# Kernel tuning notes

Hardware: AMD Instinct MI355X
Metric: run time of the kernel (lower is better)

## Reference

```python
import jax, jax.numpy as jnp
import numpy as np

V, L, D, C = 50000, 512, 300, 128
KS = (3, 4, 5)
B = 64


def setup_inputs() -> dict:
    key = jax.random.key(0)
    ks = jax.random.split(key, 12)
    inp = {
        "x": jax.random.randint(ks[0], (B, L), 0, V),
        "embed_w": jax.random.normal(ks[1], (V, D), jnp.float32) * 0.1,
        "conv_w": jax.random.normal(ks[2], (C, D), jnp.float32) * 0.05,
        "conv_b": jax.random.normal(ks[3], (C,), jnp.float32) * 0.05,
        "fc3_w": jax.random.normal(ks[4], (L - 3,), jnp.float32) * 0.04,
        "fc3_b": jax.random.normal(ks[5], (1,), jnp.float32) * 0.04,
        "fc4_w": jax.random.normal(ks[6], (L - 4,), jnp.float32) * 0.04,
        "fc4_b": jax.random.normal(ks[7], (1,), jnp.float32) * 0.04,
        "fc5_w": jax.random.normal(ks[8], (L - 5,), jnp.float32) * 0.04,
        "fc5_b": jax.random.normal(ks[9], (1,), jnp.float32) * 0.04,
        "fc_w": jax.random.normal(ks[10], (C, C * len(KS)), jnp.float32) * 0.05,
        "fc_b": jax.random.normal(ks[11], (C,), jnp.float32) * 0.05,
    }
    return inp


def reference(x, embed_w, conv_w, conv_b, fc3_w, fc3_b, fc4_w, fc4_b,
              fc5_w, fc5_b, fc_w, fc_b):
    # Embedding lookup: [B, L, D]
    emb = embed_w[x]
    # Exclusive prefix sum over the sequence dim (O(L) sliding sums).
    cs = jnp.concatenate(
        [jnp.zeros_like(emb[:, :1]), jnp.cumsum(emb, axis=1)], axis=1)  # [B, L+1, D]
    fcs = ((fc3_w, fc3_b), (fc4_w, fc4_b), (fc5_w, fc5_b))
    outs = []
    for k, (wk, bk) in zip(KS, fcs):
        # Window i sums tokens i..i+k-1; only L-k windows (range(L-k) in original).
        win = cs[:, k:L] - cs[:, :L - k]                      # [B, L-k, D]
        # conv_sim: dot each window-sum against C label vectors (kernel (1, D)).
        sim = jnp.einsum('bld,cd->bcl', win, conv_w) + conv_b[None, :, None]
        # Dropout is identity in eval; fcs[k]: Linear(L-k, 1) shared across channels.
        outs.append(jnp.einsum('bcl,l->bc', sim, wk) + bk)    # [B, C]
    h = jnp.concatenate(outs, axis=1)                          # [B, C*3]
    return h @ fc_w.T + fc_b                                   # [B, C]
```

## Files before the change

kernel.cpp:

```cpp
#include <hip/hip_runtime.h>
#include <stdint.h>

#define BB 64
#define LL 512
#define DD 300
#define CC 128

#define OFF_GRED  (BB * 32 * 3 * DD)
#define OFF_W2    (OFF_GRED + BB * 3 * DD)
#define OFF_BIAS2 (OFF_W2 + CC * 3 * DD)

__global__ __launch_bounds__(256) void k_gather(
    const int* __restrict__ x, const float* __restrict__ embed,
    const float* __restrict__ conv_w, const float* __restrict__ conv_b,
    const float* __restrict__ w3, const float* __restrict__ b3,
    const float* __restrict__ w4, const float* __restrict__ b4,
    const float* __restrict__ w5, const float* __restrict__ b5,
    const float* __restrict__ fcw, const float* __restrict__ fcb,
    float* __restrict__ Gpart, float* __restrict__ W2,
    float* __restrict__ bias2) {
  const int blk = blockIdx.x;
  const int tid = threadIdx.x;

  if (blk < 1024) {
    const int b = blk >> 4;
    const int tc = blk & 15;
    const int sub = tid >> 7;
    const int stid = tid & 127;

    __shared__ int sx[32];
    __shared__ float su[3][32];

    if (tid < 32) {
      const int t = tc * 32 + tid;
      sx[tid] = x[b * LL + t];
      const float* ws[3] = {w3, w4, w5};
#pragma unroll
      for (int kk = 0; kk < 3; ++kk) {
        const int k = kk + 3;
        int lo = t - k + 1; if (lo < 0) lo = 0;
        int hi = t; const int lim = LL - k - 1; if (hi > lim) hi = lim;
        float s = 0.f;
        for (int l = lo; l <= hi; ++l) s += ws[kk][l];
        su[kk][tid] = s;
      }
    }
    __syncthreads();

    float a0x = 0.f, a0y = 0.f, a1x = 0.f, a1y = 0.f, a2x = 0.f, a2y = 0.f;
    float c0x = 0.f, c0y = 0.f, c1x = 0.f, c1y = 0.f, c2x = 0.f, c2y = 0.f;
    const bool tail = stid < (DD / 2 - 128);

#pragma unroll
    for (int half = 0; half < 2; ++half) {
      const int base = sub * 16 + half * 8;
      float2 v[8], u[8];
#pragma unroll
      for (int i = 0; i < 8; ++i) {
        const float2* rp = (const float2*)(embed + (size_t)sx[base + i] * DD);
        v[i] = rp[stid];
      }
      if (tail) {
#pragma unroll
        for (int i = 0; i < 8; ++i) {
          const float2* rp =
              (const float2*)(embed + (size_t)sx[base + i] * DD);
          u[i] = rp[128 + stid];
        }
      }
#pragma unroll
      for (int i = 0; i < 8; ++i) {
        const int j = base + i;
        const float w0 = su[0][j], w1 = su[1][j], w2 = su[2][j];
        a0x += w0 * v[i].x; a0y += w0 * v[i].y;
        a1x += w1 * v[i].x; a1y += w1 * v[i].y;
        a2x += w2 * v[i].x; a2y += w2 * v[i].y;
        if (tail) {
          c0x += w0 * u[i].x; c0y += w0 * u[i].y;
          c1x += w1 * u[i].x; c1y += w1 * u[i].y;
          c2x += w2 * u[i].x; c2y += w2 * u[i].y;
        }
      }
    }

    const int p = tc * 2 + sub;
    float* Gp = Gpart + (size_t)(b * 32 + p) * (3 * DD);
    const int d0 = 2 * stid;
    Gp[0 * DD + d0] = a0x; Gp[0 * DD + d0 + 1] = a0y;
    Gp[1 * DD + d0] = a1x; Gp[1 * DD + d0 + 1] = a1y;
    Gp[2 * DD + d0] = a2x; Gp[2 * DD + d0 + 1] = a2y;
    if (tail) {
      const int d1 = 2 * (128 + stid);
      Gp[0 * DD + d1] = c0x; Gp[0 * DD + d1 + 1] = c0y;
      Gp[1 * DD + d1] = c1x; Gp[1 * DD + d1 + 1] = c1y;
      Gp[2 * DD + d1] = c2x; Gp[2 * DD + d1 + 1] = c2y;
    }
  } else if (blk < 1504) {
    const int w = (blk - 1024) * 4 + (tid >> 6);
    const int lane = tid & 63;
    const int c = w / 15;
    const int rem = w - c * 15;
    const int kk = rem / 5;
    const int chunk = rem - kk * 5;
    const int d = chunk * 64 + lane;
    if (d < DD) {
      const float* fr = fcw + c * (3 * CC) + kk * CC;
      float acc0 = 0.f, acc1 = 0.f;
#pragma unroll 4
      for (int cp = 0; cp < CC; cp += 2) {
        acc0 += fr[cp] * conv_w[cp * DD + d];
        acc1 += fr[cp + 1] * conv_w[(cp + 1) * DD + d];
      }
      W2[c * (3 * DD) + kk * DD + d] = acc0 + acc1;
    }
  } else {
    const int wid = tid >> 6;
    const int lane = tid & 63;
    const int c = (blk - 1504) * 4 + wid;
    float sk[3];
    const float* ws[3] = {w3, w4, w5};
#pragma unroll
    for (int kk = 0; kk < 3; ++kk) {
      const int len = LL - (kk + 3);
      float s = 0.f;
      for (int l = lane; l < len; l += 64) s += ws[kk][l];
#pragma unroll
      for (int off = 32; off >= 1; off >>= 1) s += __shfl_down(s, off, 64);
      sk[kk] = __shfl(s, 0, 64);
    }
    const float bkv[3] = {b3[0], b4[0], b5[0]};
    float acc = 0.f;
#pragma unroll
    for (int s6 = 0; s6 < 6; ++s6) {
      const int j = s6 * 64 + lane;
      const int kk = j >> 7;
      const int cp = j & 127;
      acc += fcw[c * (3 * CC) + j] * (conv_b[cp] * sk[kk] + bkv[kk]);
    }
#pragma unroll
    for (int off = 32; off >= 1; off >>= 1) acc += __shfl_down(acc, off, 64);
    if (lane == 0) bias2[c] = acc + fcb[c];
  }
}

__global__ __launch_bounds__(256) void k_reduce(
    const float* __restrict__ Gpart, float* __restrict__ Gred) {
  const int gid = blockIdx.x * 256 + threadIdx.x;
  const int o = gid >> 4;
  const int r = gid & 15;
  const int b = o / 225;
  const int q = o - b * 225;
  const float4* gp =
      (const float4*)Gpart + (size_t)b * 32 * 225 + (size_t)(2 * r) * 225 + q;
  const float4 v0 = gp[0];
  const float4 v1 = gp[225];
  float4 s;
  s.x = v0.x + v1.x; s.y = v0.y + v1.y; s.z = v0.z + v1.z; s.w = v0.w + v1.w;
#pragma unroll
  for (int off = 1; off <= 8; off <<= 1) {
    s.x += __shfl_down(s.x, off, 64);
    s.y += __shfl_down(s.y, off, 64);
    s.z += __shfl_down(s.z, off, 64);
    s.w += __shfl_down(s.w, off, 64);
  }
  if (r == 0) ((float4*)Gred)[o] = s;
}

__global__ __launch_bounds__(256) void k_out(
    const float* __restrict__ Gred, const float* __restrict__ W2,
    const float* __restrict__ bias2, float* __restrict__ out) {
  const int wg = blockIdx.x * 4 + (threadIdx.x >> 6);
  const int lane = threadIdx.x & 63;
  const int b = wg >> 6;
  const int c0 = (wg & 63) * 2;

  const float2* gr = (const float2*)(Gred + b * (3 * DD));
  const float2* wr0 = (const float2*)(W2 + c0 * (3 * DD));
  const float2* wr1 = (const float2*)(W2 + (c0 + 1) * (3 * DD));
  float a0 = 0.f, a1 = 0.f;
#pragma unroll
  for (int s = 0; s < 7; ++s) {
    const float2 g = gr[s * 64 + lane];
    const float2 va = wr0[s * 64 + lane];
    const float2 vb = wr1[s * 64 + lane];
    a0 += va.x * g.x + va.y * g.y;
    a1 += vb.x * g.x + vb.y * g.y;
  }
  if (lane < 2) {
    const float2 g = gr[448 + lane];
    const float2 va = wr0[448 + lane];
    const float2 vb = wr1[448 + lane];
    a0 += va.x * g.x + va.y * g.y;
    a1 += vb.x * g.x + vb.y * g.y;
  }
#pragma unroll
  for (int off = 32; off >= 1; off >>= 1) {
    a0 += __shfl_down(a0, off, 64);
    a1 += __shfl_down(a1, off, 64);
  }
  if (lane == 0) {
    out[b * CC + c0] = a0 + bias2[c0];
    out[b * CC + c0 + 1] = a1 + bias2[c0 + 1];
  }
}

extern "C" void kernel_launch(void* const* d_in, const int* in_sizes, int n_in,
                              void* d_out, int out_size, void* d_ws,
                              size_t ws_size, hipStream_t stream) {
  const int* x = (const int*)d_in[0];
  const float* embed = (const float*)d_in[1];
  const float* conv_w = (const float*)d_in[2];
  const float* conv_b = (const float*)d_in[3];
  const float* fc3w = (const float*)d_in[4];
  const float* fc3b = (const float*)d_in[5];
  const float* fc4w = (const float*)d_in[6];
  const float* fc4b = (const float*)d_in[7];
  const float* fc5w = (const float*)d_in[8];
  const float* fc5b = (const float*)d_in[9];
  const float* fcw = (const float*)d_in[10];
  const float* fcb = (const float*)d_in[11];

  float* Gpart = (float*)d_ws;
  float* Gred = (float*)d_ws + OFF_GRED;
  float* W2 = (float*)d_ws + OFF_W2;
  float* bias2 = (float*)d_ws + OFF_BIAS2;

  k_gather<<<dim3(1536), dim3(256), 0, stream>>>(
      x, embed, conv_w, conv_b, fc3w, fc3b, fc4w, fc4b, fc5w, fc5b, fcw, fcb,
      Gpart, W2, bias2);
  k_reduce<<<dim3(900), dim3(256), 0, stream>>>(Gpart, Gred);
  k_out<<<dim3(1024), dim3(256), 0, stream>>>(Gred, W2, bias2,
                                              (float*)d_out);
}
```

Measured before the change: 130.0 us.

## Gather embedding rows with float4 loads using 320-thread blocks and 64 partials

Each gather block now uses 320 threads, 300 of them active. They are split into 4 token groups of 8 tokens, and each thread loads a float4 slice of the 300-wide embedding row, replacing the earlier float2 split with its uneven tail path. This doubles the number of partial sums per batch to 64, so the reduce kernel now adds 4 partials per lane instead of 2. The W2 and bias block ranges are remapped to 5 waves per block. The aim is wider, fully coalesced loads with no divergent tail, at the cost of twice the partial-sum workspace traffic and 20 idle threads per gather block.

```diff
diff --git a/kernel.cpp b/kernel.cpp
--- a/kernel.cpp
+++ b/kernel.cpp
@@ -5,12 +5,13 @@
 #define LL 512
 #define DD 300
 #define CC 128
-
-#define OFF_GRED  (BB * 32 * 3 * DD)
+#define NP 64
+
+#define OFF_GRED  (BB * NP * 3 * DD)
 #define OFF_W2    (OFF_GRED + BB * 3 * DD)
 #define OFF_BIAS2 (OFF_W2 + CC * 3 * DD)
 
-__global__ __launch_bounds__(256) void k_gather(
+__global__ __launch_bounds__(320) void k_gather(
     const int* __restrict__ x, const float* __restrict__ embed,
     const float* __restrict__ conv_w, const float* __restrict__ conv_b,
     const float* __restrict__ w3, const float* __restrict__ b3,
@@ -25,8 +26,6 @@
   if (blk < 1024) {
     const int b = blk >> 4;
     const int tc = blk & 15;
-    const int sub = tid >> 7;
-    const int stid = tid & 127;
 
     __shared__ int sx[32];
     __shared__ float su[3][32];
@@ -47,56 +46,41 @@
     }
     __syncthreads();
 
-    float a0x = 0.f, a0y = 0.f, a1x = 0.f, a1y = 0.f, a2x = 0.f, a2y = 0.f;
-    float c0x = 0.f, c0y = 0.f, c1x = 0.f, c1y = 0.f, c2x = 0.f, c2y = 0.f;
-    const bool tail = stid < (DD / 2 - 128);
-
-#pragma unroll
-    for (int half = 0; half < 2; ++half) {
-      const int base = sub * 16 + half * 8;
-      float2 v[8], u[8];
+    if (tid < 300) {
+      const int tg = tid / 75;
+      const int d4 = tid - tg * 75;
+      const int i0 = tg * 8;
+
+      float4 v[8];
 #pragma unroll
       for (int i = 0; i < 8; ++i) {
-        const float2* rp = (const float2*)(embed + (size_t)sx[base + i] * DD);
-        v[i] = rp[stid];
-      }
-      if (tail) {
-#pragma unroll
-        for (int i = 0; i < 8; ++i) {
-          const float2* rp =
-              (const float2*)(embed + (size_t)sx[base + i] * DD);
-          u[i] = rp[128 + stid];
-        }
-      }
+        const float4* rp = (const float4*)(embed + (size_t)sx[i0 + i] * DD);
+        v[i] = rp[d4];
+      }
+
+      float4 a0 = {0.f, 0.f, 0.f, 0.f};
+      float4 a1 = {0.f, 0.f, 0.f, 0.f};
+      float4 a2 = {0.f, 0.f, 0.f, 0.f};
 #pragma unroll
       for (int i = 0; i < 8; ++i) {
-        const int j = base + i;
+        const int j = i0 + i;
         const float w0 = su[0][j], w1 = su[1][j], w2 = su[2][j];
-        a0x += w0 * v[i].x; a0y += w0 * v[i].y;
-        a1x += w1 * v[i].x; a1y += w1 * v[i].y;
-        a2x += w2 * v[i].x; a2y += w2 * v[i].y;
-        if (tail) {
-          c0x += w0 * u[i].x; c0y += w0 * u[i].y;
-          c1x += w1 * u[i].x; c1y += w1 * u[i].y;
-          c2x += w2 * u[i].x; c2y += w2 * u[i].y;
-        }
-      }
-    }
-
-    const int p = tc * 2 + sub;
-    float* Gp = Gpart + (size_t)(b * 32 + p) * (3 * DD);
-    const int d0 = 2 * stid;
-    Gp[0 * DD + d0] = a0x; Gp[0 * DD + d0 + 1] = a0y;
-    Gp[1 * DD + d0] = a1x; Gp[1 * DD + d0 + 1] = a1y;
-    Gp[2 * DD + d0] = a2x; Gp[2 * DD + d0 + 1] = a2y;
-    if (tail) {
-      const int d1 = 2 * (128 + stid);
-      Gp[0 * DD + d1] = c0x; Gp[0 * DD + d1 + 1] = c0y;
-      Gp[1 * DD + d1] = c1x; Gp[1 * DD + d1 + 1] = c1y;
-      Gp[2 * DD + d1] = c2x; Gp[2 * DD + d1 + 1] = c2y;
-    }
-  } else if (blk < 1504) {
-    const int w = (blk - 1024) * 4 + (tid >> 6);
+        a0.x += w0 * v[i].x; a0.y += w0 * v[i].y;
+        a0.z += w0 * v[i].z; a0.w += w0 * v[i].w;
+        a1.x += w1 * v[i].x; a1.y += w1 * v[i].y;
+        a1.z += w1 * v[i].z; a1.w += w1 * v[i].w;
+        a2.x += w2 * v[i].x; a2.y += w2 * v[i].y;
+        a2.z += w2 * v[i].z; a2.w += w2 * v[i].w;
+      }
+
+      const int p = tc * 4 + tg;
+      float* Gp = Gpart + (size_t)(b * NP + p) * (3 * DD);
+      ((float4*)(Gp + 0 * DD))[d4] = a0;
+      ((float4*)(Gp + 1 * DD))[d4] = a1;
+      ((float4*)(Gp + 2 * DD))[d4] = a2;
+    }
+  } else if (blk < 1408) {
+    const int w = (blk - 1024) * 5 + (tid >> 6);
     const int lane = tid & 63;
     const int c = w / 15;
     const int rem = w - c * 15;
@@ -116,30 +100,32 @@
   } else {
     const int wid = tid >> 6;
     const int lane = tid & 63;
-    const int c = (blk - 1504) * 4 + wid;
-    float sk[3];
-    const float* ws[3] = {w3, w4, w5};
-#pragma unroll
-    for (int kk = 0; kk < 3; ++kk) {
-      const int len = LL - (kk + 3);
-      float s = 0.f;
-      for (int l = lane; l < len; l += 64) s += ws[kk][l];
-#pragma unroll
-      for (int off = 32; off >= 1; off >>= 1) s += __shfl_down(s, off, 64);
-      sk[kk] = __shfl(s, 0, 64);
-    }
-    const float bkv[3] = {b3[0], b4[0], b5[0]};
-    float acc = 0.f;
-#pragma unroll
-    for (int s6 = 0; s6 < 6; ++s6) {
-      const int j = s6 * 64 + lane;
-      const int kk = j >> 7;
-      const int cp = j & 127;
-      acc += fcw[c * (3 * CC) + j] * (conv_b[cp] * sk[kk] + bkv[kk]);
-    }
-#pragma unroll
-    for (int off = 32; off >= 1; off >>= 1) acc += __shfl_down(acc, off, 64);
-    if (lane == 0) bias2[c] = acc + fcb[c];
+    const int c = (blk - 1408) * 5 + wid;
+    if (c < CC) {
+      float sk[3];
+      const float* ws[3] = {w3, w4, w5};
+#pragma unroll
+      for (int kk = 0; kk < 3; ++kk) {
+        const int len = LL - (kk + 3);
+        float s = 0.f;
+        for (int l = lane; l < len; l += 64) s += ws[kk][l];
+#pragma unroll
+        for (int off = 32; off >= 1; off >>= 1) s += __shfl_down(s, off, 64);
+        sk[kk] = __shfl(s, 0, 64);
+      }
+      const float bkv[3] = {b3[0], b4[0], b5[0]};
+      float acc = 0.f;
+#pragma unroll
+      for (int s6 = 0; s6 < 6; ++s6) {
+        const int j = s6 * 64 + lane;
+        const int kk = j >> 7;
+        const int cp = j & 127;
+        acc += fcw[c * (3 * CC) + j] * (conv_b[cp] * sk[kk] + bkv[kk]);
+      }
+#pragma unroll
+      for (int off = 32; off >= 1; off >>= 1) acc += __shfl_down(acc, off, 64);
+      if (lane == 0) bias2[c] = acc + fcb[c];
+    }
   }
 }
 
@@ -151,11 +137,16 @@
   const int b = o / 225;
   const int q = o - b * 225;
   const float4* gp =
-      (const float4*)Gpart + (size_t)b * 32 * 225 + (size_t)(2 * r) * 225 + q;
+      (const float4*)Gpart + ((size_t)b * NP + r * 4) * 225 + q;
   const float4 v0 = gp[0];
   const float4 v1 = gp[225];
+  const float4 v2 = gp[450];
+  const float4 v3 = gp[675];
   float4 s;
-  s.x = v0.x + v1.x; s.y = v0.y + v1.y; s.z = v0.z + v1.z; s.w = v0.w + v1.w;
+  s.x = (v0.x + v1.x) + (v2.x + v3.x);
+  s.y = (v0.y + v1.y) + (v2.y + v3.y);
+  s.z = (v0.z + v1.z) + (v2.z + v3.z);
+  s.w = (v0.w + v1.w) + (v2.w + v3.w);
 #pragma unroll
   for (int off = 1; off <= 8; off <<= 1) {
     s.x += __shfl_down(s.x, off, 64);
@@ -225,7 +216,7 @@
   float* W2 = (float*)d_ws + OFF_W2;
   float* bias2 = (float*)d_ws + OFF_BIAS2;
 
-  k_gather<<<dim3(1536), dim3(256), 0, stream>>>(
+  k_gather<<<dim3(1434), dim3(320), 0, stream>>>(
       x, embed, conv_w, conv_b, fc3w, fc3b, fc4w, fc4b, fc5w, fc5b, fcw, fcb,
       Gpart, W2, bias2);
   k_reduce<<<dim3(900), dim3(256), 0, stream>>>(Gpart, Gred);
```

Measured after the change: 131.3 us. No clear change (+1.0%).
